# Optimization experiments

Measured on AMD Instinct MI355X. Metric: run time of the kernel, lower is better.

Reference implementation:

```python
import jax, jax.numpy as jnp
import numpy as np

B, S, D, H = 8, 1024, 768, 12
DH = D // H  # 64


def setup_inputs() -> dict:
    key = jax.random.key(0)
    ks = jax.random.split(key, 7)
    scale = 0.05
    return {
        "sequences": jax.random.normal(ks[0], (B, S, D), dtype=jnp.float32),
        "Wq": jax.random.normal(ks[1], (H, DH, DH), dtype=jnp.float32) * scale,
        "bq": jax.random.normal(ks[2], (H, DH), dtype=jnp.float32) * scale,
        "Wk": jax.random.normal(ks[3], (H, DH, DH), dtype=jnp.float32) * scale,
        "bk": jax.random.normal(ks[4], (H, DH), dtype=jnp.float32) * scale,
        "Wv": jax.random.normal(ks[5], (H, DH, DH), dtype=jnp.float32) * scale,
        "bv": jax.random.normal(ks[6], (H, DH), dtype=jnp.float32) * scale,
    }


def reference(sequences, Wq, bq, Wk, bk, Wv, bv):
    # sequences: [B, S, D]; per-head slice of width DH gets its own Linear.
    b, s, d = sequences.shape
    h, dh = Wq.shape[0], Wq.shape[-1]
    xh = sequences.reshape(b, s, h, dh)  # [B,S,H,DH] head-chunked features
    q = jnp.einsum('bshd,hde->bshe', xh, Wq) + bq  # [B,S,H,DH]
    k = jnp.einsum('bshd,hde->bshe', xh, Wk) + bk
    v = jnp.einsum('bshd,hde->bshe', xh, Wv) + bv
    scores = jnp.einsum('bqhd,bkhd->bhqk', q, k) / jnp.sqrt(jnp.float32(dh))
    weights = jax.nn.softmax(scores, axis=-1)  # [B,H,S,S]
    out = jnp.einsum('bhqk,bkhd->bqhd', weights, v)  # [B,S,H,DH]
    return out.reshape(b, s, d)  # hstack of heads == reshape back to D
```

## Files before the change

### kernel.cpp

```cpp
#include <hip/hip_runtime.h>
#include <hip/hip_bf16.h>
#include <math.h>

constexpr int Bn = 8, Sn = 1024, Dn = 768, Hn = 12, DHn = 64;
constexpr int QKV_ELEMS = Bn * Hn * Sn * DHn;
constexpr float SQC = 0.42466086f;

typedef __attribute__((ext_vector_type(8))) short bf16x8;
typedef __attribute__((ext_vector_type(4))) float f32x4;

__device__ __forceinline__ unsigned short f2bf(float f) {
    union { float f; unsigned u; } c{f};
    return (unsigned short)((c.u + 0x8000) >> 16);
}
__device__ __forceinline__ unsigned int pk2bf(float a, float b) {
    union { float f; unsigned u; } ca{a}, cb{b};
    return __builtin_amdgcn_perm(cb.u + 0x8000u, ca.u + 0x8000u, 0x07060302u);
}

__device__ __forceinline__ bf16x8 wfrag(const float* __restrict__ W,
                                        int e, int kc, int quad, float sc) {
    const float* p = W + (size_t)(kc * 32 + quad * 8) * 64 + e;
    unsigned int tmp[4];
    #pragma unroll
    for (int j = 0; j < 4; j++)
        tmp[j] = pk2bf(p[(2 * j) * 64] * sc, p[(2 * j + 1) * 64] * sc);
    return *(bf16x8*)tmp;
}

__global__ __launch_bounds__(256) void proj_kernel(
    const float* __restrict__ x,
    const float* __restrict__ Wk, const float* __restrict__ bk,
    const float* __restrict__ Wv, const float* __restrict__ bv,
    unsigned short* __restrict__ k_ws, unsigned short* __restrict__ vt_ws)
{
    __shared__ unsigned short Xs[64 * 72];
    __shared__ unsigned short ObK[64 * 72];
    __shared__ unsigned short ObV[64 * 72];

    const int blk  = blockIdx.x;
    const int tile = blk & 15;
    const int bh   = blk >> 4;
    const int h    = bh % Hn;
    const int b    = bh / Hn;
    const int t    = threadIdx.x;
    const int w    = t >> 6;
    const int lane = t & 63;
    const int l    = lane & 15;
    const int quad = lane >> 4;
    const int sr   = t >> 2;
    const int sc0  = (t & 3) * 16;
    const int s0   = tile * 64;

    {
        const float* xrow = x + ((size_t)(b * Sn + s0 + sr) * Dn + h * 64 + sc0);
        unsigned int tmp[8];
        #pragma unroll
        for (int q4 = 0; q4 < 4; q4++) {
            float4 v = ((const float4*)xrow)[q4];
            tmp[2 * q4 + 0] = pk2bf(v.x, v.y);
            tmp[2 * q4 + 1] = pk2bf(v.z, v.w);
        }
        *(uint4*)&Xs[sr * 72 + sc0]     = ((uint4*)tmp)[0];
        *(uint4*)&Xs[sr * 72 + sc0 + 8] = ((uint4*)tmp)[1];
    }

    const int e = w * 16 + l;
    bf16x8 wk[2], wv[2];
    #pragma unroll
    for (int kc = 0; kc < 2; kc++) {
        wk[kc] = wfrag(Wk + (size_t)h * 4096, e, kc, quad, SQC);
        wv[kc] = wfrag(Wv + (size_t)h * 4096, e, kc, quad, 1.0f);
    }
    float4 bkv = *(const float4*)(bk + h * 64 + w * 16 + quad * 4);
    bkv.x *= SQC; bkv.y *= SQC; bkv.z *= SQC; bkv.w *= SQC;
    const float bvl = bv[h * 64 + e];

    __syncthreads();

    bf16x8 xf[4][2];
    #pragma unroll
    for (int nt = 0; nt < 4; nt++)
        #pragma unroll
        for (int kc = 0; kc < 2; kc++)
            xf[nt][kc] = *(bf16x8*)&Xs[(nt * 16 + l) * 72 + kc * 32 + quad * 8];

    #pragma unroll
    for (int nt = 0; nt < 4; nt++) {
        f32x4 ak = (f32x4){bkv.x, bkv.y, bkv.z, bkv.w};
        ak = __builtin_amdgcn_mfma_f32_16x16x32_bf16(wk[0], xf[nt][0], ak, 0, 0, 0);
        ak = __builtin_amdgcn_mfma_f32_16x16x32_bf16(wk[1], xf[nt][1], ak, 0, 0, 0);
        *(uint2*)&ObK[(nt * 16 + l) * 72 + w * 16 + quad * 4] =
            make_uint2(pk2bf(ak[0], ak[1]), pk2bf(ak[2], ak[3]));
        f32x4 av = (f32x4){bvl, bvl, bvl, bvl};
        av = __builtin_amdgcn_mfma_f32_16x16x32_bf16(xf[nt][0], wv[0], av, 0, 0, 0);
        av = __builtin_amdgcn_mfma_f32_16x16x32_bf16(xf[nt][1], wv[1], av, 0, 0, 0);
        *(uint2*)&ObV[(w * 16 + l) * 72 + nt * 16 + quad * 4] =
            make_uint2(pk2bf(av[0], av[1]), pk2bf(av[2], av[3]));
    }
    __syncthreads();

    {
        uint4 a  = *(uint4*)&ObK[sr * 72 + sc0];
        uint4 b4 = *(uint4*)&ObK[sr * 72 + sc0 + 8];
        unsigned short* dst = k_ws + (size_t)(bh * Sn + s0 + sr) * 64 + sc0;
        ((uint4*)dst)[0] = a;
        *(uint4*)(dst + 8) = b4;
    }
    {
        uint4 a  = *(uint4*)&ObV[sr * 72 + sc0];
        uint4 b4 = *(uint4*)&ObV[sr * 72 + sc0 + 8];
        unsigned short* dst = vt_ws + (size_t)bh * 64 * Sn + (size_t)sr * Sn + s0 + sc0;
        ((uint4*)dst)[0] = a;
        *(uint4*)(dst + 8) = b4;
    }
}

__global__ __launch_bounds__(256) void attn_kernel(
    const float* __restrict__ x,
    const float* __restrict__ Wq, const float* __restrict__ bq,
    const unsigned short* __restrict__ k_ws,
    const unsigned short* __restrict__ vt_ws,
    float* __restrict__ out)
{
    __shared__ unsigned short Ks[64 * 72];
    __shared__ unsigned short Vt[64 * 72];
    __shared__ unsigned short Pws[4 * 32 * 72];

    const int blk = blockIdx.x;
    const int xcd = blk & 7;
    const int idx = blk >> 3;
    const int bh  = xcd * 12 + (idx % 12);
    const int qt  = idx / 12;
    const int t    = threadIdx.x;
    const int w    = t >> 6;
    const int lane = t & 63;
    const int l    = lane & 15;
    const int quad = lane >> 4;
    const int sr   = t >> 2;
    const int sc0  = (t & 3) * 16;

    const int b = bh / Hn, h = bh % Hn;
    const size_t base  = (size_t)bh * Sn * 64;
    const size_t vbase = (size_t)bh * 64 * Sn;
    unsigned short* Pw = Pws + w * 32 * 72;

    bf16x8 qf[2][2];
    {
        bf16x8 xq[2][2];
        #pragma unroll
        for (int st = 0; st < 2; st++) {
            const float* xp = x + ((size_t)(b * Sn + qt * 128 + w * 32 + st * 16 + l) * Dn
                                   + h * 64 + quad * 8);
            #pragma unroll
            for (int kc = 0; kc < 2; kc++) {
                float4 v0 = *(const float4*)(xp + kc * 32);
                float4 v1 = *(const float4*)(xp + kc * 32 + 4);
                unsigned int tmp[4] = {pk2bf(v0.x, v0.y), pk2bf(v0.z, v0.w),
                                       pk2bf(v1.x, v1.y), pk2bf(v1.z, v1.w)};
                xq[st][kc] = *(bf16x8*)tmp;
            }
        }
        #pragma unroll
        for (int nt = 0; nt < 4; nt++) {
            bf16x8 wa0 = wfrag(Wq + (size_t)h * 4096, nt * 16 + l, 0, quad, SQC);
            bf16x8 wa1 = wfrag(Wq + (size_t)h * 4096, nt * 16 + l, 1, quad, SQC);
            float4 bqv = *(const float4*)(bq + h * 64 + nt * 16 + quad * 4);
            #pragma unroll
            for (int st = 0; st < 2; st++) {
                f32x4 acc = (f32x4){bqv.x * SQC, bqv.y * SQC, bqv.z * SQC, bqv.w * SQC};
                acc = __builtin_amdgcn_mfma_f32_16x16x32_bf16(wa0, xq[st][0], acc, 0, 0, 0);
                acc = __builtin_amdgcn_mfma_f32_16x16x32_bf16(wa1, xq[st][1], acc, 0, 0, 0);
                *(uint2*)&Pw[(st * 16 + l) * 72 + nt * 16 + quad * 4] =
                    make_uint2(pk2bf(acc[0], acc[1]), pk2bf(acc[2], acc[3]));
            }
        }
        __asm__ volatile("s_waitcnt lgkmcnt(0)" ::: "memory");
        #pragma unroll
        for (int st = 0; st < 2; st++) {
            qf[st][0] = *(bf16x8*)&Pw[(st * 16 + l) * 72 + quad * 8];
            qf[st][1] = *(bf16x8*)&Pw[(st * 16 + l) * 72 + 32 + quad * 8];
        }
    }

    f32x4 Oa[2][4];
    #pragma unroll
    for (int st = 0; st < 2; st++)
        #pragma unroll
        for (int nt = 0; nt < 4; nt++) Oa[st][nt] = (f32x4){0.f, 0.f, 0.f, 0.f};
    float ps[2] = {0.f, 0.f};

    uint4 kpre0, kpre1, vpre0, vpre1;
    {
        const unsigned short* kp = k_ws + base + (size_t)sr * 64 + sc0;
        kpre0 = *(const uint4*)kp;
        kpre1 = *(const uint4*)(kp + 8);
        const unsigned short* vp = vt_ws + vbase + (size_t)sr * Sn + sc0;
        vpre0 = *(const uint4*)vp;
        vpre1 = *(const uint4*)(vp + 8);
    }

    for (int kt = 0; kt < 16; kt++) {
        __syncthreads();
        {
            *(uint4*)&Ks[sr * 72 + sc0]     = kpre0;
            *(uint4*)&Ks[sr * 72 + sc0 + 8] = kpre1;
            *(uint4*)&Vt[sr * 72 + sc0]     = vpre0;
            *(uint4*)&Vt[sr * 72 + sc0 + 8] = vpre1;
        }
        __syncthreads();

        if (kt + 1 < 16) {
            const unsigned short* kp = k_ws + base + (size_t)((kt + 1) * 64 + sr) * 64 + sc0;
            kpre0 = *(const uint4*)kp;
            kpre1 = *(const uint4*)(kp + 8);
            const unsigned short* vp = vt_ws + vbase + (size_t)sr * Sn + (kt + 1) * 64 + sc0;
            vpre0 = *(const uint4*)vp;
            vpre1 = *(const uint4*)(vp + 8);
        }

        #pragma unroll
        for (int nt = 0; nt < 4; nt++) {
            bf16x8 kf0 = *(bf16x8*)&Ks[(nt * 16 + l) * 72 + quad * 8];
            bf16x8 kf1 = *(bf16x8*)&Ks[(nt * 16 + l) * 72 + 32 + quad * 8];
            #pragma unroll
            for (int st = 0; st < 2; st++) {
                f32x4 s = (f32x4){0.f, 0.f, 0.f, 0.f};
                s = __builtin_amdgcn_mfma_f32_16x16x32_bf16(kf0, qf[st][0], s, 0, 0, 0);
                s = __builtin_amdgcn_mfma_f32_16x16x32_bf16(kf1, qf[st][1], s, 0, 0, 0);
                float p0 = exp2f(s[0]), p1 = exp2f(s[1]);
                float p2 = exp2f(s[2]), p3 = exp2f(s[3]);
                ps[st] += (p0 + p1) + (p2 + p3);
                *(uint2*)&Pw[(st * 16 + l) * 72 + nt * 16 + quad * 4] =
                    make_uint2(pk2bf(p0, p1), pk2bf(p2, p3));
            }
        }
        __asm__ volatile("s_waitcnt lgkmcnt(0)" ::: "memory");

        bf16x8 pf[2][2];
        #pragma unroll
        for (int st = 0; st < 2; st++) {
            pf[st][0] = *(bf16x8*)&Pw[(st * 16 + l) * 72 + quad * 8];
            pf[st][1] = *(bf16x8*)&Pw[(st * 16 + l) * 72 + 32 + quad * 8];
        }

        #pragma unroll
        for (int nt = 0; nt < 4; nt++) {
            bf16x8 vf0 = *(bf16x8*)&Vt[(nt * 16 + l) * 72 + quad * 8];
            bf16x8 vf1 = *(bf16x8*)&Vt[(nt * 16 + l) * 72 + 32 + quad * 8];
            #pragma unroll
            for (int st = 0; st < 2; st++) {
                Oa[st][nt] = __builtin_amdgcn_mfma_f32_16x16x32_bf16(pf[st][0], vf0, Oa[st][nt], 0, 0, 0);
                Oa[st][nt] = __builtin_amdgcn_mfma_f32_16x16x32_bf16(pf[st][1], vf1, Oa[st][nt], 0, 0, 0);
            }
        }
    }

    #pragma unroll
    for (int st = 0; st < 2; st++) {
        ps[st] += __shfl_xor(ps[st], 16, 64);
        ps[st] += __shfl_xor(ps[st], 32, 64);
    }
    #pragma unroll
    for (int st = 0; st < 2; st++) {
        float inv[4];
        #pragma unroll
        for (int r = 0; r < 4; r++) inv[r] = 1.0f / __shfl(ps[st], quad * 4 + r, 64);
        #pragma unroll
        for (int nt = 0; nt < 4; nt++)
            #pragma unroll
            for (int r = 0; r < 4; r++) {
                int srow = qt * 128 + w * 32 + st * 16 + quad * 4 + r;
                out[(size_t)(b * Sn + srow) * Dn + h * 64 + nt * 16 + l] = Oa[st][nt][r] * inv[r];
            }
    }
}

extern "C" void kernel_launch(void* const* d_in, const int* in_sizes, int n_in,
                              void* d_out, int out_size, void* d_ws, size_t ws_size,
                              hipStream_t stream) {
    const float* x  = (const float*)d_in[0];
    const float* Wq = (const float*)d_in[1];
    const float* bq = (const float*)d_in[2];
    const float* Wk = (const float*)d_in[3];
    const float* bk = (const float*)d_in[4];
    const float* Wv = (const float*)d_in[5];
    const float* bv = (const float*)d_in[6];
    float* out = (float*)d_out;

    unsigned short* k_ws  = (unsigned short*)d_ws;
    unsigned short* vt_ws = k_ws + QKV_ELEMS;

    hipLaunchKernelGGL(proj_kernel, dim3(Bn * Hn * 16), dim3(256), 0, stream,
                       x, Wk, bk, Wv, bv, k_ws, vt_ws);
    hipLaunchKernelGGL(attn_kernel, dim3(Bn * Hn * 8), dim3(256), 0, stream,
                       x, Wq, bq, k_ws, vt_ws, out);
}
```

Baseline: 139.6 us.

## Fuse K/V projection into attention kernel, recomputing per key tile

```diff
diff --git a/kernel.cpp b/kernel.cpp
--- a/kernel.cpp
+++ b/kernel.cpp
@@ -3,16 +3,11 @@
 #include <math.h>
 
 constexpr int Bn = 8, Sn = 1024, Dn = 768, Hn = 12, DHn = 64;
-constexpr int QKV_ELEMS = Bn * Hn * Sn * DHn;
 constexpr float SQC = 0.42466086f;
 
 typedef __attribute__((ext_vector_type(8))) short bf16x8;
 typedef __attribute__((ext_vector_type(4))) float f32x4;
 
-__device__ __forceinline__ unsigned short f2bf(float f) {
-    union { float f; unsigned u; } c{f};
-    return (unsigned short)((c.u + 0x8000) >> 16);
-}
 __device__ __forceinline__ unsigned int pk2bf(float a, float b) {
     union { float f; unsigned u; } ca{a}, cb{b};
     return __builtin_amdgcn_perm(cb.u + 0x8000u, ca.u + 0x8000u, 0x07060302u);
@@ -28,101 +23,14 @@
     return *(bf16x8*)tmp;
 }
 
-__global__ __launch_bounds__(256) void proj_kernel(
+__global__ __launch_bounds__(256, 3) void mhsa_fused_kernel(
     const float* __restrict__ x,
+    const float* __restrict__ Wq, const float* __restrict__ bq,
     const float* __restrict__ Wk, const float* __restrict__ bk,
     const float* __restrict__ Wv, const float* __restrict__ bv,
-    unsigned short* __restrict__ k_ws, unsigned short* __restrict__ vt_ws)
+    float* __restrict__ out)
 {
     __shared__ unsigned short Xs[64 * 72];
-    __shared__ unsigned short ObK[64 * 72];
-    __shared__ unsigned short ObV[64 * 72];
-
-    const int blk  = blockIdx.x;
-    const int tile = blk & 15;
-    const int bh   = blk >> 4;
-    const int h    = bh % Hn;
-    const int b    = bh / Hn;
-    const int t    = threadIdx.x;
-    const int w    = t >> 6;
-    const int lane = t & 63;
-    const int l    = lane & 15;
-    const int quad = lane >> 4;
-    const int sr   = t >> 2;
-    const int sc0  = (t & 3) * 16;
-    const int s0   = tile * 64;
-
-    {
-        const float* xrow = x + ((size_t)(b * Sn + s0 + sr) * Dn + h * 64 + sc0);
-        unsigned int tmp[8];
-        #pragma unroll
-        for (int q4 = 0; q4 < 4; q4++) {
-            float4 v = ((const float4*)xrow)[q4];
-            tmp[2 * q4 + 0] = pk2bf(v.x, v.y);
-            tmp[2 * q4 + 1] = pk2bf(v.z, v.w);
-        }
-        *(uint4*)&Xs[sr * 72 + sc0]     = ((uint4*)tmp)[0];
-        *(uint4*)&Xs[sr * 72 + sc0 + 8] = ((uint4*)tmp)[1];
-    }
-
-    const int e = w * 16 + l;
-    bf16x8 wk[2], wv[2];
-    #pragma unroll
-    for (int kc = 0; kc < 2; kc++) {
-        wk[kc] = wfrag(Wk + (size_t)h * 4096, e, kc, quad, SQC);
-        wv[kc] = wfrag(Wv + (size_t)h * 4096, e, kc, quad, 1.0f);
-    }
-    float4 bkv = *(const float4*)(bk + h * 64 + w * 16 + quad * 4);
-    bkv.x *= SQC; bkv.y *= SQC; bkv.z *= SQC; bkv.w *= SQC;
-    const float bvl = bv[h * 64 + e];
-
-    __syncthreads();
-
-    bf16x8 xf[4][2];
-    #pragma unroll
-    for (int nt = 0; nt < 4; nt++)
-        #pragma unroll
-        for (int kc = 0; kc < 2; kc++)
-            xf[nt][kc] = *(bf16x8*)&Xs[(nt * 16 + l) * 72 + kc * 32 + quad * 8];
-
-    #pragma unroll
-    for (int nt = 0; nt < 4; nt++) {
-        f32x4 ak = (f32x4){bkv.x, bkv.y, bkv.z, bkv.w};
-        ak = __builtin_amdgcn_mfma_f32_16x16x32_bf16(wk[0], xf[nt][0], ak, 0, 0, 0);
-        ak = __builtin_amdgcn_mfma_f32_16x16x32_bf16(wk[1], xf[nt][1], ak, 0, 0, 0);
-        *(uint2*)&ObK[(nt * 16 + l) * 72 + w * 16 + quad * 4] =
-            make_uint2(pk2bf(ak[0], ak[1]), pk2bf(ak[2], ak[3]));
-        f32x4 av = (f32x4){bvl, bvl, bvl, bvl};
-        av = __builtin_amdgcn_mfma_f32_16x16x32_bf16(xf[nt][0], wv[0], av, 0, 0, 0);
-        av = __builtin_amdgcn_mfma_f32_16x16x32_bf16(xf[nt][1], wv[1], av, 0, 0, 0);
-        *(uint2*)&ObV[(w * 16 + l) * 72 + nt * 16 + quad * 4] =
-            make_uint2(pk2bf(av[0], av[1]), pk2bf(av[2], av[3]));
-    }
-    __syncthreads();
-
-    {
-        uint4 a  = *(uint4*)&ObK[sr * 72 + sc0];
-        uint4 b4 = *(uint4*)&ObK[sr * 72 + sc0 + 8];
-        unsigned short* dst = k_ws + (size_t)(bh * Sn + s0 + sr) * 64 + sc0;
-        ((uint4*)dst)[0] = a;
-        *(uint4*)(dst + 8) = b4;
-    }
-    {
-        uint4 a  = *(uint4*)&ObV[sr * 72 + sc0];
-        uint4 b4 = *(uint4*)&ObV[sr * 72 + sc0 + 8];
-        unsigned short* dst = vt_ws + (size_t)bh * 64 * Sn + (size_t)sr * Sn + s0 + sc0;
-        ((uint4*)dst)[0] = a;
-        *(uint4*)(dst + 8) = b4;
-    }
-}
-
-__global__ __launch_bounds__(256) void attn_kernel(
-    const float* __restrict__ x,
-    const float* __restrict__ Wq, const float* __restrict__ bq,
-    const unsigned short* __restrict__ k_ws,
-    const unsigned short* __restrict__ vt_ws,
-    float* __restrict__ out)
-{
     __shared__ unsigned short Ks[64 * 72];
     __shared__ unsigned short Vt[64 * 72];
     __shared__ unsigned short Pws[4 * 32 * 72];
@@ -141,9 +49,24 @@
     const int sc0  = (t & 3) * 16;
 
     const int b = bh / Hn, h = bh % Hn;
-    const size_t base  = (size_t)bh * Sn * 64;
-    const size_t vbase = (size_t)bh * 64 * Sn;
     unsigned short* Pw = Pws + w * 32 * 72;
+    const float* xh = x + (size_t)b * Sn * Dn + h * 64;
+
+    const int e = w * 16 + l;
+    bf16x8 wkf[2], wvf[2];
+    #pragma unroll
+    for (int kc = 0; kc < 2; kc++) {
+        wkf[kc] = wfrag(Wk + (size_t)h * 4096, e, kc, quad, SQC);
+        wvf[kc] = wfrag(Wv + (size_t)h * 4096, e, kc, quad, 1.0f);
+    }
+    float4 bkv = *(const float4*)(bk + h * 64 + w * 16 + quad * 4);
+    bkv.x *= SQC; bkv.y *= SQC; bkv.z *= SQC; bkv.w *= SQC;
+    const float bvl = bv[h * 64 + e];
+
+    float4 rx[4];
+    #pragma unroll
+    for (int q4 = 0; q4 < 4; q4++)
+        rx[q4] = ((const float4*)(xh + (size_t)sr * Dn + sc0))[q4];
 
     bf16x8 qf[2][2];
     {
@@ -183,6 +106,42 @@
         }
     }
 
+    {
+        unsigned int tmp[8];
+        #pragma unroll
+        for (int q4 = 0; q4 < 4; q4++) {
+            tmp[2 * q4]     = pk2bf(rx[q4].x, rx[q4].y);
+            tmp[2 * q4 + 1] = pk2bf(rx[q4].z, rx[q4].w);
+        }
+        *(uint4*)&Xs[sr * 72 + sc0]     = ((uint4*)tmp)[0];
+        *(uint4*)&Xs[sr * 72 + sc0 + 8] = ((uint4*)tmp)[1];
+    }
+    __syncthreads();
+
+    uint2 kpk[4], vpk[4];
+    {
+        bf16x8 xf[4][2];
+        #pragma unroll
+        for (int nt = 0; nt < 4; nt++)
+            #pragma unroll
+            for (int kc = 0; kc < 2; kc++)
+                xf[nt][kc] = *(bf16x8*)&Xs[(nt * 16 + l) * 72 + kc * 32 + quad * 8];
+        #pragma unroll
+        for (int nt = 0; nt < 4; nt++) {
+            f32x4 ak = (f32x4){bkv.x, bkv.y, bkv.z, bkv.w};
+            ak = __builtin_amdgcn_mfma_f32_16x16x32_bf16(wkf[0], xf[nt][0], ak, 0, 0, 0);
+            ak = __builtin_amdgcn_mfma_f32_16x16x32_bf16(wkf[1], xf[nt][1], ak, 0, 0, 0);
+            kpk[nt] = make_uint2(pk2bf(ak[0], ak[1]), pk2bf(ak[2], ak[3]));
+            f32x4 av = (f32x4){bvl, bvl, bvl, bvl};
+            av = __builtin_amdgcn_mfma_f32_16x16x32_bf16(xf[nt][0], wvf[0], av, 0, 0, 0);
+            av = __builtin_amdgcn_mfma_f32_16x16x32_bf16(xf[nt][1], wvf[1], av, 0, 0, 0);
+            vpk[nt] = make_uint2(pk2bf(av[0], av[1]), pk2bf(av[2], av[3]));
+        }
+    }
+    #pragma unroll
+    for (int q4 = 0; q4 < 4; q4++)
+        rx[q4] = ((const float4*)(xh + (size_t)(64 + sr) * Dn + sc0))[q4];
+
     f32x4 Oa[2][4];
     #pragma unroll
     for (int st = 0; st < 2; st++)
@@ -190,33 +149,48 @@
         for (int nt = 0; nt < 4; nt++) Oa[st][nt] = (f32x4){0.f, 0.f, 0.f, 0.f};
     float ps[2] = {0.f, 0.f};
 
-    uint4 kpre0, kpre1, vpre0, vpre1;
-    {
-        const unsigned short* kp = k_ws + base + (size_t)sr * 64 + sc0;
-        kpre0 = *(const uint4*)kp;
-        kpre1 = *(const uint4*)(kp + 8);
-        const unsigned short* vp = vt_ws + vbase + (size_t)sr * Sn + sc0;
-        vpre0 = *(const uint4*)vp;
-        vpre1 = *(const uint4*)(vp + 8);
-    }
-
     for (int kt = 0; kt < 16; kt++) {
         __syncthreads();
-        {
-            *(uint4*)&Ks[sr * 72 + sc0]     = kpre0;
-            *(uint4*)&Ks[sr * 72 + sc0 + 8] = kpre1;
-            *(uint4*)&Vt[sr * 72 + sc0]     = vpre0;
-            *(uint4*)&Vt[sr * 72 + sc0 + 8] = vpre1;
+        #pragma unroll
+        for (int nt = 0; nt < 4; nt++) {
+            *(uint2*)&Ks[(nt * 16 + l) * 72 + w * 16 + quad * 4] = kpk[nt];
+            *(uint2*)&Vt[(w * 16 + l) * 72 + nt * 16 + quad * 4] = vpk[nt];
+        }
+        if (kt < 15) {
+            unsigned int tmp[8];
+            #pragma unroll
+            for (int q4 = 0; q4 < 4; q4++) {
+                tmp[2 * q4]     = pk2bf(rx[q4].x, rx[q4].y);
+                tmp[2 * q4 + 1] = pk2bf(rx[q4].z, rx[q4].w);
+            }
+            *(uint4*)&Xs[sr * 72 + sc0]     = ((uint4*)tmp)[0];
+            *(uint4*)&Xs[sr * 72 + sc0 + 8] = ((uint4*)tmp)[1];
         }
         __syncthreads();
 
-        if (kt + 1 < 16) {
-            const unsigned short* kp = k_ws + base + (size_t)((kt + 1) * 64 + sr) * 64 + sc0;
-            kpre0 = *(const uint4*)kp;
-            kpre1 = *(const uint4*)(kp + 8);
-            const unsigned short* vp = vt_ws + vbase + (size_t)sr * Sn + (kt + 1) * 64 + sc0;
-            vpre0 = *(const uint4*)vp;
-            vpre1 = *(const uint4*)(vp + 8);
+        if (kt < 14) {
+            #pragma unroll
+            for (int q4 = 0; q4 < 4; q4++)
+                rx[q4] = ((const float4*)(xh + (size_t)((kt + 2) * 64 + sr) * Dn + sc0))[q4];
+        }
+        if (kt < 15) {
+            bf16x8 xf[4][2];
+            #pragma unroll
+            for (int nt = 0; nt < 4; nt++)
+                #pragma unroll
+                for (int kc = 0; kc < 2; kc++)
+                    xf[nt][kc] = *(bf16x8*)&Xs[(nt * 16 + l) * 72 + kc * 32 + quad * 8];
+            #pragma unroll
+            for (int nt = 0; nt < 4; nt++) {
+                f32x4 ak = (f32x4){bkv.x, bkv.y, bkv.z, bkv.w};
+                ak = __builtin_amdgcn_mfma_f32_16x16x32_bf16(wkf[0], xf[nt][0], ak, 0, 0, 0);
+                ak = __builtin_amdgcn_mfma_f32_16x16x32_bf16(wkf[1], xf[nt][1], ak, 0, 0, 0);
+                kpk[nt] = make_uint2(pk2bf(ak[0], ak[1]), pk2bf(ak[2], ak[3]));
+                f32x4 av = (f32x4){bvl, bvl, bvl, bvl};
+                av = __builtin_amdgcn_mfma_f32_16x16x32_bf16(xf[nt][0], wvf[0], av, 0, 0, 0);
+                av = __builtin_amdgcn_mfma_f32_16x16x32_bf16(xf[nt][1], wvf[1], av, 0, 0, 0);
+                vpk[nt] = make_uint2(pk2bf(av[0], av[1]), pk2bf(av[2], av[3]));
+            }
         }
 
         #pragma unroll
@@ -286,13 +260,7 @@
     const float* bk = (const float*)d_in[4];
     const float* Wv = (const float*)d_in[5];
     const float* bv = (const float*)d_in[6];
-    float* out = (float*)d_out;
-
-    unsigned short* k_ws  = (unsigned short*)d_ws;
-    unsigned short* vt_ws = k_ws + QKV_ELEMS;
-
-    hipLaunchKernelGGL(proj_kernel, dim3(Bn * Hn * 16), dim3(256), 0, stream,
-                       x, Wk, bk, Wv, bv, k_ws, vt_ws);
-    hipLaunchKernelGGL(attn_kernel, dim3(Bn * Hn * 8), dim3(256), 0, stream,
-                       x, Wq, bq, k_ws, vt_ws, out);
-}
+
+    hipLaunchKernelGGL(mhsa_fused_kernel, dim3(Bn * Hn * 8), dim3(256), 0, stream,
+                       x, Wq, bq, Wk, bk, Wv, bv, (float*)d_out);
+}
```

After: 152.1 us. 1.09x slower.

## Load K/V MFMA fragments directly from global memory, drop LDS staging and barriers

Applied to the files above, without the earlier changes.

```diff
diff --git a/kernel.cpp b/kernel.cpp
--- a/kernel.cpp
+++ b/kernel.cpp
@@ -9,10 +9,6 @@
 typedef __attribute__((ext_vector_type(8))) short bf16x8;
 typedef __attribute__((ext_vector_type(4))) float f32x4;
 
-__device__ __forceinline__ unsigned short f2bf(float f) {
-    union { float f; unsigned u; } c{f};
-    return (unsigned short)((c.u + 0x8000) >> 16);
-}
 __device__ __forceinline__ unsigned int pk2bf(float a, float b) {
     union { float f; unsigned u; } ca{a}, cb{b};
     return __builtin_amdgcn_perm(cb.u + 0x8000u, ca.u + 0x8000u, 0x07060302u);
@@ -39,8 +35,10 @@
     __shared__ unsigned short ObV[64 * 72];
 
     const int blk  = blockIdx.x;
-    const int tile = blk & 15;
-    const int bh   = blk >> 4;
+    const int xcd  = blk & 7;
+    const int g    = blk >> 3;
+    const int bh   = xcd * 12 + (g % 12);
+    const int tile = g / 12;
     const int h    = bh % Hn;
     const int b    = bh / Hn;
     const int t    = threadIdx.x;
@@ -116,15 +114,13 @@
     }
 }
 
-__global__ __launch_bounds__(256) void attn_kernel(
+__global__ __launch_bounds__(256, 3) void attn_kernel(
     const float* __restrict__ x,
     const float* __restrict__ Wq, const float* __restrict__ bq,
     const unsigned short* __restrict__ k_ws,
     const unsigned short* __restrict__ vt_ws,
     float* __restrict__ out)
 {
-    __shared__ unsigned short Ks[64 * 72];
-    __shared__ unsigned short Vt[64 * 72];
     __shared__ unsigned short Pws[4 * 32 * 72];
 
     const int blk = blockIdx.x;
@@ -137,8 +133,6 @@
     const int lane = t & 63;
     const int l    = lane & 15;
     const int quad = lane >> 4;
-    const int sr   = t >> 2;
-    const int sc0  = (t & 3) * 16;
 
     const int b = bh / Hn, h = bh % Hn;
     const size_t base  = (size_t)bh * Sn * 64;
@@ -190,44 +184,27 @@
         for (int nt = 0; nt < 4; nt++) Oa[st][nt] = (f32x4){0.f, 0.f, 0.f, 0.f};
     float ps[2] = {0.f, 0.f};
 
-    uint4 kpre0, kpre1, vpre0, vpre1;
-    {
-        const unsigned short* kp = k_ws + base + (size_t)sr * 64 + sc0;
-        kpre0 = *(const uint4*)kp;
-        kpre1 = *(const uint4*)(kp + 8);
-        const unsigned short* vp = vt_ws + vbase + (size_t)sr * Sn + sc0;
-        vpre0 = *(const uint4*)vp;
-        vpre1 = *(const uint4*)(vp + 8);
-    }
-
     for (int kt = 0; kt < 16; kt++) {
-        __syncthreads();
-        {
-            *(uint4*)&Ks[sr * 72 + sc0]     = kpre0;
-            *(uint4*)&Ks[sr * 72 + sc0 + 8] = kpre1;
-            *(uint4*)&Vt[sr * 72 + sc0]     = vpre0;
-            *(uint4*)&Vt[sr * 72 + sc0 + 8] = vpre1;
-        }
-        __syncthreads();
-
-        if (kt + 1 < 16) {
-            const unsigned short* kp = k_ws + base + (size_t)((kt + 1) * 64 + sr) * 64 + sc0;
-            kpre0 = *(const uint4*)kp;
-            kpre1 = *(const uint4*)(kp + 8);
-            const unsigned short* vp = vt_ws + vbase + (size_t)sr * Sn + (kt + 1) * 64 + sc0;
-            vpre0 = *(const uint4*)vp;
-            vpre1 = *(const uint4*)(vp + 8);
-        }
-
-        #pragma unroll
-        for (int nt = 0; nt < 4; nt++) {
-            bf16x8 kf0 = *(bf16x8*)&Ks[(nt * 16 + l) * 72 + quad * 8];
-            bf16x8 kf1 = *(bf16x8*)&Ks[(nt * 16 + l) * 72 + 32 + quad * 8];
+        bf16x8 kf[4][2], vf[4][2];
+        #pragma unroll
+        for (int nt = 0; nt < 4; nt++) {
+            const unsigned short* kp =
+                k_ws + base + (size_t)(kt * 64 + nt * 16 + l) * 64 + quad * 8;
+            kf[nt][0] = *(const bf16x8*)kp;
+            kf[nt][1] = *(const bf16x8*)(kp + 32);
+            const unsigned short* vp =
+                vt_ws + vbase + (size_t)(nt * 16 + l) * Sn + kt * 64 + quad * 8;
+            vf[nt][0] = *(const bf16x8*)vp;
+            vf[nt][1] = *(const bf16x8*)(vp + 32);
+        }
+
+        #pragma unroll
+        for (int nt = 0; nt < 4; nt++) {
             #pragma unroll
             for (int st = 0; st < 2; st++) {
                 f32x4 s = (f32x4){0.f, 0.f, 0.f, 0.f};
-                s = __builtin_amdgcn_mfma_f32_16x16x32_bf16(kf0, qf[st][0], s, 0, 0, 0);
-                s = __builtin_amdgcn_mfma_f32_16x16x32_bf16(kf1, qf[st][1], s, 0, 0, 0);
+                s = __builtin_amdgcn_mfma_f32_16x16x32_bf16(kf[nt][0], qf[st][0], s, 0, 0, 0);
+                s = __builtin_amdgcn_mfma_f32_16x16x32_bf16(kf[nt][1], qf[st][1], s, 0, 0, 0);
                 float p0 = exp2f(s[0]), p1 = exp2f(s[1]);
                 float p2 = exp2f(s[2]), p3 = exp2f(s[3]);
                 ps[st] += (p0 + p1) + (p2 + p3);
@@ -246,12 +223,10 @@
 
         #pragma unroll
         for (int nt = 0; nt < 4; nt++) {
-            bf16x8 vf0 = *(bf16x8*)&Vt[(nt * 16 + l) * 72 + quad * 8];
-            bf16x8 vf1 = *(bf16x8*)&Vt[(nt * 16 + l) * 72 + 32 + quad * 8];
             #pragma unroll
             for (int st = 0; st < 2; st++) {
-                Oa[st][nt] = __builtin_amdgcn_mfma_f32_16x16x32_bf16(pf[st][0], vf0, Oa[st][nt], 0, 0, 0);
-                Oa[st][nt] = __builtin_amdgcn_mfma_f32_16x16x32_bf16(pf[st][1], vf1, Oa[st][nt], 0, 0, 0);
+                Oa[st][nt] = __builtin_amdgcn_mfma_f32_16x16x32_bf16(pf[st][0], vf[nt][0], Oa[st][nt], 0, 0, 0);
+                Oa[st][nt] = __builtin_amdgcn_mfma_f32_16x16x32_bf16(pf[st][1], vf[nt][1], Oa[st][nt], 0, 0, 0);
             }
         }
     }
```

Result: slower. 189.0 us (+35.3%).

## Replace LDS round-trip for Q and P fragments with in-register lane shuffles

Applied to the files above, without the earlier changes.

```diff
diff --git a/kernel.cpp b/kernel.cpp
--- a/kernel.cpp
+++ b/kernel.cpp
@@ -9,13 +9,20 @@
 typedef __attribute__((ext_vector_type(8))) short bf16x8;
 typedef __attribute__((ext_vector_type(4))) float f32x4;
 
-__device__ __forceinline__ unsigned short f2bf(float f) {
-    union { float f; unsigned u; } c{f};
-    return (unsigned short)((c.u + 0x8000) >> 16);
-}
 __device__ __forceinline__ unsigned int pk2bf(float a, float b) {
     union { float f; unsigned u; } ca{a}, cb{b};
     return __builtin_amdgcn_perm(cb.u + 0x8000u, ca.u + 0x8000u, 0x07060302u);
+}
+
+__device__ __forceinline__ void quad_net(unsigned &X, unsigned &Y, int quad) {
+    unsigned v = (quad >= 2) ? X : Y;
+    v = __shfl_xor(v, 32, 64);
+    unsigned X1 = (quad >= 2) ? v : X;
+    unsigned Y1 = (quad >= 2) ? Y : v;
+    unsigned w2 = (quad & 1) ? X1 : Y1;
+    w2 = __shfl_xor(w2, 16, 64);
+    X = (quad & 1) ? w2 : X1;
+    Y = (quad & 1) ? Y1 : w2;
 }
 
 __device__ __forceinline__ bf16x8 wfrag(const float* __restrict__ W,
@@ -39,8 +46,10 @@
     __shared__ unsigned short ObV[64 * 72];
 
     const int blk  = blockIdx.x;
-    const int tile = blk & 15;
-    const int bh   = blk >> 4;
+    const int xcd  = blk & 7;
+    const int g    = blk >> 3;
+    const int bh   = xcd * 12 + (g % 12);
+    const int tile = g / 12;
     const int h    = bh % Hn;
     const int b    = bh / Hn;
     const int t    = threadIdx.x;
@@ -116,7 +125,7 @@
     }
 }
 
-__global__ __launch_bounds__(256) void attn_kernel(
+__global__ __launch_bounds__(256, 3) void attn_kernel(
     const float* __restrict__ x,
     const float* __restrict__ Wq, const float* __restrict__ bq,
     const unsigned short* __restrict__ k_ws,
@@ -125,7 +134,6 @@
 {
     __shared__ unsigned short Ks[64 * 72];
     __shared__ unsigned short Vt[64 * 72];
-    __shared__ unsigned short Pws[4 * 32 * 72];
 
     const int blk = blockIdx.x;
     const int xcd = blk & 7;
@@ -143,7 +151,6 @@
     const int b = bh / Hn, h = bh % Hn;
     const size_t base  = (size_t)bh * Sn * 64;
     const size_t vbase = (size_t)bh * 64 * Sn;
-    unsigned short* Pw = Pws + w * 32 * 72;
 
     bf16x8 qf[2][2];
     {
@@ -161,6 +168,7 @@
                 xq[st][kc] = *(bf16x8*)tmp;
             }
         }
+        unsigned qq[2][4][2];
         #pragma unroll
         for (int nt = 0; nt < 4; nt++) {
             bf16x8 wa0 = wfrag(Wq + (size_t)h * 4096, nt * 16 + l, 0, quad, SQC);
@@ -171,16 +179,21 @@
                 f32x4 acc = (f32x4){bqv.x * SQC, bqv.y * SQC, bqv.z * SQC, bqv.w * SQC};
                 acc = __builtin_amdgcn_mfma_f32_16x16x32_bf16(wa0, xq[st][0], acc, 0, 0, 0);
                 acc = __builtin_amdgcn_mfma_f32_16x16x32_bf16(wa1, xq[st][1], acc, 0, 0, 0);
-                *(uint2*)&Pw[(st * 16 + l) * 72 + nt * 16 + quad * 4] =
-                    make_uint2(pk2bf(acc[0], acc[1]), pk2bf(acc[2], acc[3]));
-            }
-        }
-        __asm__ volatile("s_waitcnt lgkmcnt(0)" ::: "memory");
-        #pragma unroll
-        for (int st = 0; st < 2; st++) {
-            qf[st][0] = *(bf16x8*)&Pw[(st * 16 + l) * 72 + quad * 8];
-            qf[st][1] = *(bf16x8*)&Pw[(st * 16 + l) * 72 + 32 + quad * 8];
-        }
+                qq[st][nt][0] = pk2bf(acc[0], acc[1]);
+                qq[st][nt][1] = pk2bf(acc[2], acc[3]);
+            }
+        }
+        #pragma unroll
+        for (int st = 0; st < 2; st++)
+            #pragma unroll
+            for (int kc = 0; kc < 2; kc++) {
+                unsigned t0 = qq[st][2 * kc][0], u0 = qq[st][2 * kc + 1][0];
+                unsigned t1 = qq[st][2 * kc][1], u1 = qq[st][2 * kc + 1][1];
+                quad_net(t0, u0, quad);
+                quad_net(t1, u1, quad);
+                unsigned tmp[4] = {t0, t1, u0, u1};
+                qf[st][kc] = *(bf16x8*)tmp;
+            }
     }
 
     f32x4 Oa[2][4];
@@ -219,6 +232,7 @@
             vpre1 = *(const uint4*)(vp + 8);
         }
 
+        unsigned pp[2][4][2];
         #pragma unroll
         for (int nt = 0; nt < 4; nt++) {
             bf16x8 kf0 = *(bf16x8*)&Ks[(nt * 16 + l) * 72 + quad * 8];
@@ -231,18 +245,23 @@
                 float p0 = exp2f(s[0]), p1 = exp2f(s[1]);
                 float p2 = exp2f(s[2]), p3 = exp2f(s[3]);
                 ps[st] += (p0 + p1) + (p2 + p3);
-                *(uint2*)&Pw[(st * 16 + l) * 72 + nt * 16 + quad * 4] =
-                    make_uint2(pk2bf(p0, p1), pk2bf(p2, p3));
-            }
-        }
-        __asm__ volatile("s_waitcnt lgkmcnt(0)" ::: "memory");
-
-        bf16x8 pf[2][2];
-        #pragma unroll
-        for (int st = 0; st < 2; st++) {
-            pf[st][0] = *(bf16x8*)&Pw[(st * 16 + l) * 72 + quad * 8];
-            pf[st][1] = *(bf16x8*)&Pw[(st * 16 + l) * 72 + 32 + quad * 8];
-        }
+                pp[st][nt][0] = pk2bf(p0, p1);
+                pp[st][nt][1] = pk2bf(p2, p3);
+            }
+        }
+
+        bf16x8 pb[2][2];
+        #pragma unroll
+        for (int st = 0; st < 2; st++)
+            #pragma unroll
+            for (int kc = 0; kc < 2; kc++) {
+                unsigned t0 = pp[st][2 * kc][0], u0 = pp[st][2 * kc + 1][0];
+                unsigned t1 = pp[st][2 * kc][1], u1 = pp[st][2 * kc + 1][1];
+                quad_net(t0, u0, quad);
+                quad_net(t1, u1, quad);
+                unsigned tmp[4] = {t0, t1, u0, u1};
+                pb[st][kc] = *(bf16x8*)tmp;
+            }
 
         #pragma unroll
         for (int nt = 0; nt < 4; nt++) {
@@ -250,8 +269,8 @@
             bf16x8 vf1 = *(bf16x8*)&Vt[(nt * 16 + l) * 72 + 32 + quad * 8];
             #pragma unroll
             for (int st = 0; st < 2; st++) {
-                Oa[st][nt] = __builtin_amdgcn_mfma_f32_16x16x32_bf16(pf[st][0], vf0, Oa[st][nt], 0, 0, 0);
-                Oa[st][nt] = __builtin_amdgcn_mfma_f32_16x16x32_bf16(pf[st][1], vf1, Oa[st][nt], 0, 0, 0);
+                Oa[st][nt] = __builtin_amdgcn_mfma_f32_16x16x32_bf16(vf0, pb[st][0], Oa[st][nt], 0, 0, 0);
+                Oa[st][nt] = __builtin_amdgcn_mfma_f32_16x16x32_bf16(vf1, pb[st][1], Oa[st][nt], 0, 0, 0);
             }
         }
     }
@@ -260,19 +279,14 @@
     for (int st = 0; st < 2; st++) {
         ps[st] += __shfl_xor(ps[st], 16, 64);
         ps[st] += __shfl_xor(ps[st], 32, 64);
-    }
-    #pragma unroll
-    for (int st = 0; st < 2; st++) {
-        float inv[4];
-        #pragma unroll
-        for (int r = 0; r < 4; r++) inv[r] = 1.0f / __shfl(ps[st], quad * 4 + r, 64);
-        #pragma unroll
-        for (int nt = 0; nt < 4; nt++)
-            #pragma unroll
-            for (int r = 0; r < 4; r++) {
-                int srow = qt * 128 + w * 32 + st * 16 + quad * 4 + r;
-                out[(size_t)(b * Sn + srow) * Dn + h * 64 + nt * 16 + l] = Oa[st][nt][r] * inv[r];
-            }
+        const float inv = 1.0f / ps[st];
+        const int srow = qt * 128 + w * 32 + st * 16 + l;
+        #pragma unroll
+        for (int nt = 0; nt < 4; nt++) {
+            float4 o = make_float4(Oa[st][nt][0] * inv, Oa[st][nt][1] * inv,
+                                   Oa[st][nt][2] * inv, Oa[st][nt][3] * inv);
+            *(float4*)&out[(size_t)(b * Sn + srow) * Dn + h * 64 + nt * 16 + quad * 4] = o;
+        }
     }
 }
 
```

Measured after the change: 145.0 us. +3.8%, slower.
